# Kernel tuning notes

Measured on AMD Instinct MI355X. Metric: run time of the kernel, lower is better.

The kernel has to match this reference:

```python
import jax, jax.numpy as jnp
import numpy as np

B, T, D, H = 4, 2048, 1024, 16
HD = D // H  # 64
FF = 4 * D


def layernorm(x, g, b, eps=1e-5):
    mu = jnp.mean(x, axis=-1, keepdims=True)
    var = jnp.mean(jnp.square(x - mu), axis=-1, keepdims=True)
    return (x - mu) * jax.lax.rsqrt(var + eps) * g + b


def setup_inputs() -> dict:
    key = jax.random.key(0)
    ks = jax.random.split(key, 12)
    s_in = 1.0 / np.sqrt(D)
    s_ff = 1.0 / np.sqrt(FF)
    return {
        "x": jax.random.normal(ks[0], (B, T, D), dtype=jnp.float32),
        "mask": jnp.tril(jnp.ones((T, T), dtype=jnp.int32)),  # causal
        "ln1_g": jnp.ones((D,), jnp.float32),
        "ln1_b": jnp.zeros((D,), jnp.float32),
        "Wq": jax.random.uniform(ks[1], (H, D, HD), jnp.float32, -s_in, s_in),
        "bq": jnp.zeros((H, HD), jnp.float32),
        "Wk": jax.random.uniform(ks[2], (H, D, HD), jnp.float32, -s_in, s_in),
        "bk": jnp.zeros((H, HD), jnp.float32),
        "Wv": jax.random.uniform(ks[3], (H, D, HD), jnp.float32, -s_in, s_in),
        "bv": jnp.zeros((H, HD), jnp.float32),
        "Wo": jax.random.uniform(ks[4], (D, D), jnp.float32, -s_in, s_in),
        "bo": jnp.zeros((D,), jnp.float32),
        "ln2_g": jnp.ones((D,), jnp.float32),
        "ln2_b": jnp.zeros((D,), jnp.float32),
        "W1": jax.random.uniform(ks[5], (D, FF), jnp.float32, -s_in, s_in),
        "b1": jnp.zeros((FF,), jnp.float32),
        "W2": jax.random.uniform(ks[6], (FF, D), jnp.float32, -s_ff, s_ff),
        "b2": jnp.zeros((D,), jnp.float32),
    }


def reference(x, mask, ln1_g, ln1_b, Wq, bq, Wk, bk, Wv, bv, Wo, bo,
              ln2_g, ln2_b, W1, b1, W2, b2):
    # --- attention branch (dropout p=0, eval mode) ---
    h = layernorm(x, ln1_g, ln1_b)                      # [B,T,D]
    q = jnp.einsum('btd,hdk->bhtk', h, Wq) + bq[:, None, :]
    k = jnp.einsum('btd,hdk->bhtk', h, Wk) + bk[:, None, :]
    v = jnp.einsum('btd,hdk->bhtk', h, Wv) + bv[:, None, :]
    scores = jnp.einsum('bhqk,bhsk->bhqs', q, k) / jnp.sqrt(jnp.float32(HD))
    scores = jnp.where(mask == 0, -jnp.inf, scores)     # [B,H,T,T]
    attn = jax.nn.softmax(scores, axis=-1)
    ctx = jnp.einsum('bhqs,bhsk->bhqk', attn, v)        # [B,H,T,HD]
    # concat heads along feature dim (head order preserved)
    ctx = jnp.transpose(ctx, (0, 2, 1, 3)).reshape(x.shape[0], x.shape[1], D)
    attn_out = ctx @ Wo + bo
    x = x + attn_out
    # --- GELU FFN branch (torch nn.GELU default = exact erf) ---
    h2 = layernorm(x, ln2_g, ln2_b)
    ff = jax.nn.gelu(h2 @ W1 + b1, approximate=False) @ W2 + b2
    return x + ff
```

## Files before the change

### kernel.cpp

```cpp
#include <hip/hip_runtime.h>
#include <cstdint>
#include <cstddef>

typedef __bf16 bf16x8 __attribute__((ext_vector_type(8)));
typedef float  floatx4 __attribute__((ext_vector_type(4)));

__device__ __forceinline__ uint16_t f2b(float f) {
    uint32_t u = __builtin_bit_cast(uint32_t, f);
    return (uint16_t)((u + 0x7fffu + ((u >> 16) & 1)) >> 16);
}

__device__ __forceinline__ uint16_t bf16bits(float f) {
    __bf16 h = (__bf16)f;
    return __builtin_bit_cast(uint16_t, h);
}

__device__ __forceinline__ void gload_lds16(const void* g, void* l) {
    __builtin_amdgcn_global_load_lds(
        (__attribute__((address_space(1))) void*)(void*)g,
        (__attribute__((address_space(3))) void*)l, 16, 0, 0);
}

template<int CTRL>
__device__ __forceinline__ float dpp_rot(float v) {
    return __builtin_bit_cast(float,
        __builtin_amdgcn_update_dpp(0, __builtin_bit_cast(int, v),
                                    CTRL, 0xf, 0xf, true));
}
__device__ __forceinline__ float rowmax16(float v) {
    v = fmaxf(v, dpp_rot<0x128>(v));
    v = fmaxf(v, dpp_rot<0x124>(v));
    v = fmaxf(v, dpp_rot<0x122>(v));
    v = fmaxf(v, dpp_rot<0x121>(v));
    return v;
}
__device__ __forceinline__ float rowsum16(float v) {
    v += dpp_rot<0x128>(v);
    v += dpp_rot<0x124>(v);
    v += dpp_rot<0x122>(v);
    v += dpp_rot<0x121>(v);
    return v;
}

#define QSCALE 0.18033688011112042f

__global__ __launch_bounds__(256) void repack_qkv(
    const float* __restrict__ Wq, const float* __restrict__ Wk,
    const float* __restrict__ Wv, uint16_t* __restrict__ out)
{
    __shared__ uint16_t tile[32][33];
    const int m = blockIdx.z >> 4, h = blockIdx.z & 15;
    const float* W = (m == 0) ? Wq : (m == 1) ? Wk : Wv;
    const float scl = (m == 0) ? QSCALE : 1.0f;
    const float* src = W + (size_t)h * 1024 * 64;
    const int d0 = blockIdx.x * 32, hd0 = blockIdx.y * 32;
    const int tx = threadIdx.x & 31, ty = threadIdx.x >> 5;
#pragma unroll
    for (int i = 0; i < 4; ++i)
        tile[ty + i * 8][tx] = f2b(src[(size_t)(d0 + ty + i * 8) * 64 + hd0 + tx] * scl);
    __syncthreads();
    uint16_t* dst = out + (size_t)(m * 1024 + h * 64) * 1024;
#pragma unroll
    for (int i = 0; i < 4; ++i)
        dst[(size_t)(hd0 + ty + i * 8) * 1024 + d0 + tx] = tile[tx][ty + i * 8];
}

__global__ __launch_bounds__(256) void transpose_f2b(
    const float* __restrict__ in, uint16_t* __restrict__ out, int R, int C)
{
    __shared__ uint16_t tile[32][33];
    const int c0 = blockIdx.x * 32, r0 = blockIdx.y * 32;
    const int tx = threadIdx.x & 31, ty = threadIdx.x >> 5;
#pragma unroll
    for (int i = 0; i < 4; ++i)
        tile[ty + i * 8][tx] = f2b(in[(size_t)(r0 + ty + i * 8) * C + c0 + tx]);
    __syncthreads();
#pragma unroll
    for (int i = 0; i < 4; ++i)
        out[(size_t)(c0 + ty + i * 8) * R + r0 + tx] = tile[tx][ty + i * 8];
}

__global__ void concat_bias(const float* __restrict__ bq, const float* __restrict__ bk,
                            const float* __restrict__ bv, float* __restrict__ out)
{
    int i = blockIdx.x * 256 + threadIdx.x;
    out[i] = (i < 1024) ? bq[i] * QSCALE : (i < 2048) ? bk[i - 1024] : bv[i - 2048];
}

__global__ __launch_bounds__(256) void transpose_v(
    const uint16_t* __restrict__ qkv, uint16_t* __restrict__ Vt)
{
    __shared__ uint16_t tile[32][33];
    const int bh = blockIdx.z;
    const int b = bh >> 4, h = bh & 15;
    const int t0 = blockIdx.x * 32, hd0 = blockIdx.y * 32;
    const int tx = threadIdx.x & 31, ty = threadIdx.x >> 5;
    const uint16_t* src = qkv + (size_t)b * 2048 * 3072 + 2048 + h * 64;
#pragma unroll
    for (int i = 0; i < 4; ++i)
        tile[ty + i * 8][tx] = src[(size_t)(t0 + ty + i * 8) * 3072 + hd0 + tx];
    __syncthreads();
    uint16_t* dst = Vt + (size_t)bh * 64 * 2048;
#pragma unroll
    for (int i = 0; i < 4; ++i)
        dst[(size_t)(hd0 + ty + i * 8) * 2048 + t0 + tx] = tile[tx][ty + i * 8];
}

__global__ __launch_bounds__(256) void ln_bf16(
    const float* __restrict__ x, const float* __restrict__ g,
    const float* __restrict__ b, uint16_t* __restrict__ out)
{
    const int row = blockIdx.x;
    const int t = threadIdx.x;
    const float4 v = ((const float4*)(x + (size_t)row * 1024))[t];
    float s  = v.x + v.y + v.z + v.w;
    float s2 = v.x * v.x + v.y * v.y + v.z * v.z + v.w * v.w;
#pragma unroll
    for (int o = 32; o > 0; o >>= 1) { s += __shfl_down(s, o); s2 += __shfl_down(s2, o); }
    __shared__ float red[8];
    const int wave = t >> 6, lane = t & 63;
    if (lane == 0) { red[wave] = s; red[4 + wave] = s2; }
    __syncthreads();
    if (t == 0) {
        float a  = red[0] + red[1] + red[2] + red[3];
        float a2 = red[4] + red[5] + red[6] + red[7];
        float mu = a * (1.0f / 1024.0f);
        red[0] = mu;
        red[4] = rsqrtf(a2 * (1.0f / 1024.0f) - mu * mu + 1e-5f);
    }
    __syncthreads();
    const float mu = red[0], rs = red[4];
    const float4 gv = ((const float4*)g)[t];
    const float4 bv = ((const float4*)b)[t];
    ushort4 ov;
    ov.x = f2b((v.x - mu) * rs * gv.x + bv.x);
    ov.y = f2b((v.y - mu) * rs * gv.y + bv.y);
    ov.z = f2b((v.z - mu) * rs * gv.z + bv.z);
    ov.w = f2b((v.w - mu) * rs * gv.w + bv.w);
    ((ushort4*)(out + (size_t)row * 1024))[t] = ov;
}

__global__ __launch_bounds__(256, 3) void gemm_bf16(
    const uint16_t* __restrict__ A, const uint16_t* __restrict__ Bt,
    int M, int N, int K,
    const float* __restrict__ bias, const float* __restrict__ resid,
    float* __restrict__ outF, uint16_t* __restrict__ outB, int mode)
{
    __shared__ __align__(16) uint16_t lds[128 * 128];
    uint16_t* lA = lds;
    uint16_t* lB = lds + 128 * 64;
    const int tid  = threadIdx.x;
    const int wave = tid >> 6, lane = tid & 63;

    const int lid = (int)blockIdx.y * (int)gridDim.x + (int)blockIdx.x;
    const int xcd = lid & 7, t = lid >> 3;
    const int Mb = (M >> 7) >> 3;
    const int perChunk = Mb * 8;
    const int ch = t / perChunk, j = t - ch * perChunk;
    const int m0 = (xcd * Mb + (j & (Mb - 1))) * 128;
    const int n0 = (ch * 8 + (j / Mb)) * 128;

    const int wm = (wave >> 1) * 64, wn = (wave & 1) * 64;
    const int quad = lane >> 4, lrow = lane & 15;
    const int wbase = wave * 64;

    floatx4 acc[4][4] = {};

    const uint16_t* aT = A  + (size_t)m0 * K;
    const uint16_t* bT = Bt + (size_t)n0 * K;

    for (int k0 = 0; k0 < K; k0 += 64) {
        __syncthreads();
#pragma unroll
        for (int i = 0; i < 4; ++i) {
            const int cw = i * 256 + wbase;
            const int q  = cw + lane;
            const int row = q >> 3;
            const int g = ((q & 7) ^ (row & 7)) * 8;
            gload_lds16(aT + (size_t)row * K + k0 + g, &lA[cw * 8]);
            gload_lds16(bT + (size_t)row * K + k0 + g, &lB[cw * 8]);
        }
        __syncthreads();
        bf16x8 af[4][2], bfr[4][2];
#pragma unroll
        for (int mi = 0; mi < 4; ++mi) {
            const int rr = wm + mi * 16 + lrow;
#pragma unroll
            for (int hh = 0; hh < 2; ++hh)
                af[mi][hh] = *(const bf16x8*)
                    &lA[rr * 64 + (((hh * 4 + quad) ^ (rr & 7)) * 8)];
        }
#pragma unroll
        for (int ni = 0; ni < 4; ++ni) {
            const int rr = wn + ni * 16 + lrow;
#pragma unroll
            for (int hh = 0; hh < 2; ++hh)
                bfr[ni][hh] = *(const bf16x8*)
                    &lB[rr * 64 + (((hh * 4 + quad) ^ (rr & 7)) * 8)];
        }
#pragma unroll
        for (int mi = 0; mi < 4; ++mi)
#pragma unroll
            for (int ni = 0; ni < 4; ++ni) {
                acc[mi][ni] = __builtin_amdgcn_mfma_f32_16x16x32_bf16(
                    af[mi][0], bfr[ni][0], acc[mi][ni], 0, 0, 0);
                acc[mi][ni] = __builtin_amdgcn_mfma_f32_16x16x32_bf16(
                    af[mi][1], bfr[ni][1], acc[mi][ni], 0, 0, 0);
            }
    }

    __syncthreads();
    const int r0 = (lane >> 4) * 4;

    if (mode == 1) {
        float* cf = (float*)lds;
#pragma unroll
        for (int p = 0; p < 2; ++p) {
            if ((wave >> 1) == p) {
#pragma unroll
                for (int ni = 0; ni < 4; ++ni) {
                    const int col = wn + ni * 16 + lrow;
                    const float bv = bias[n0 + col];
#pragma unroll
                    for (int mi = 0; mi < 4; ++mi)
#pragma unroll
                        for (int r = 0; r < 4; ++r) {
                            const int row = mi * 16 + r0 + r;
                            const int g = (col >> 2) ^ (((row >> 2) & 1) << 2);
                            cf[row * 128 + g * 4 + (col & 3)] = acc[mi][ni][r] + bv;
                        }
                }
            }
            __syncthreads();
#pragma unroll
            for (int i = 0; i < 8; ++i) {
                const int ci = i * 256 + tid;
                const int row = ci >> 5, cg = ci & 31;
                const int g = cg ^ (((row >> 2) & 1) << 2);
                float4 v = *(const float4*)&cf[row * 128 + g * 4];
                const size_t gidx = (size_t)(m0 + p * 64 + row) * N + n0 + cg * 4;
                const float4 rz = *(const float4*)&resid[gidx];
                v.x += rz.x; v.y += rz.y; v.z += rz.z; v.w += rz.w;
                *(float4*)&outF[gidx] = v;
            }
            __syncthreads();
        }
    } else {
#pragma unroll
        for (int ni = 0; ni < 4; ++ni) {
            const int col = wn + ni * 16 + lrow;
            const float bv = bias[n0 + col];
#pragma unroll
            for (int mi = 0; mi < 4; ++mi)
#pragma unroll
                for (int r = 0; r < 4; ++r) {
                    const int row = wm + mi * 16 + r0 + r;
                    float v = acc[mi][ni][r] + bv;
                    if (mode == 2)
                        v = 0.5f * v * (1.0f + erff(v * 0.70710678118654752f));
                    const int g = (col >> 3) ^ (((row >> 2) & 3) << 1);
                    lds[row * 128 + g * 8 + (col & 7)] = bf16bits(v);
                }
        }
        __syncthreads();
#pragma unroll
        for (int i = 0; i < 8; ++i) {
            const int ci = i * 256 + tid;
            const int row = ci >> 4, cg = ci & 15;
            const int g = cg ^ (((row >> 2) & 3) << 1);
            const bf16x8 v = *(const bf16x8*)&lds[row * 128 + g * 8];
            *(bf16x8*)&outB[(size_t)(m0 + row) * N + n0 + cg * 8] = v;
        }
    }
}

__global__ __launch_bounds__(256, 2) void attn_kernel(
    const uint16_t* __restrict__ qkv, const uint16_t* __restrict__ Vt,
    uint16_t* __restrict__ ctx)
{
    const int h = blockIdx.y, b = blockIdx.z;
    const int tid = threadIdx.x, wave = tid >> 6, lane = tid & 63;
    const int quad = lane >> 4, lcol = lane & 15, lr4 = quad * 4;
    const int sx = lcol & 7;
    const uint16_t* qbase = qkv + (size_t)b * 2048 * 3072;
    const uint16_t* kgb = qbase + 1024 + h * 64;
    const uint16_t* vtb = Vt + (size_t)(b * 16 + h) * 64 * 2048;

    __shared__ __align__(16) uint16_t kbuf[2][64 * 64];
    __shared__ __align__(16) uint16_t vbuf[2][64 * 64];
    __shared__ __align__(16) uint16_t pshm[4][32 * 64];

    const int rr = lane >> 3, sl = lane & 7;
    const int swz = sl ^ rr;

#define STAGE(ktile, bb)                                                        \
    {                                                                           \
        const int _kb = (ktile) * 64;                                           \
        _Pragma("unroll")                                                       \
        for (int i = 0; i < 2; ++i) {                                           \
            const int j = wave * 2 + i;                                         \
            const int r = j * 8 + rr;                                           \
            gload_lds16(kgb + (size_t)(_kb + r) * 3072 + swz * 8,               \
                        &kbuf[bb][j * 512]);                                    \
            gload_lds16(vtb + (size_t)r * 2048 + _kb + swz * 8,                 \
                        &vbuf[bb][j * 512]);                                    \
        }                                                                       \
    }

    for (int pp = 0; pp < 2; ++pp) {
        const int qt = pp ? (int)blockIdx.x : 15 - (int)blockIdx.x;
        const int qr0 = qt * 128 + wave * 32;

        bf16x8 qf[2][2];
#pragma unroll
        for (int mi = 0; mi < 2; ++mi) {
            const uint16_t* qp = qbase + (size_t)(qr0 + mi * 16 + lcol) * 3072 + h * 64;
            qf[mi][0] = *(const bf16x8*)(qp + quad * 8);
            qf[mi][1] = *(const bf16x8*)(qp + 32 + quad * 8);
        }

        floatx4 o[2][4] = {};
        float m_i[2][4], l_i[2][4];
#pragma unroll
        for (int mi = 0; mi < 2; ++mi)
#pragma unroll
            for (int r = 0; r < 4; ++r) { m_i[mi][r] = -1e30f; l_i[mi][r] = 0.f; }

        const int nk = 2 * qt + 2;
        __syncthreads();
        STAGE(0, 0);
        int cur = 0;

        for (int kt = 0; kt < nk; ++kt) {
            const int kb = kt * 64;
            __syncthreads();
            if (kt + 1 < nk) STAGE(kt + 1, cur ^ 1);

            if (kb <= qr0 + 31) {
                bf16x8 kf[4][2];
#pragma unroll
                for (int nt = 0; nt < 4; ++nt) {
                    const int krow = nt * 16 + lcol;
                    kf[nt][0] = *(const bf16x8*)&kbuf[cur][krow * 64 + ((quad ^ sx) * 8)];
                    kf[nt][1] = *(const bf16x8*)&kbuf[cur][krow * 64 + (((quad + 4) ^ sx) * 8)];
                }
#pragma unroll
                for (int mi = 0; mi < 2; ++mi) {
                    floatx4 sv[4];
#pragma unroll
                    for (int nt = 0; nt < 4; ++nt) {
                        floatx4 s = {0.f, 0.f, 0.f, 0.f};
                        s = __builtin_amdgcn_mfma_f32_16x16x32_bf16(qf[mi][0], kf[nt][0], s, 0, 0, 0);
                        s = __builtin_amdgcn_mfma_f32_16x16x32_bf16(qf[mi][1], kf[nt][1], s, 0, 0, 0);
                        sv[nt] = s;
                    }
                    if (kb + 63 > qr0 + mi * 16) {
#pragma unroll
                        for (int nt = 0; nt < 4; ++nt)
#pragma unroll
                            for (int r = 0; r < 4; ++r) {
                                const int row = qr0 + mi * 16 + lr4 + r;
                                const int col = kb + nt * 16 + lcol;
                                if (col > row) sv[nt][r] = -1e30f;
                            }
                    }
#pragma unroll
                    for (int r = 0; r < 4; ++r) {
                        float m = fmaxf(fmaxf(sv[0][r], sv[1][r]),
                                        fmaxf(sv[2][r], sv[3][r]));
                        m = rowmax16(m);
                        const float mn = fmaxf(m_i[mi][r], m);
                        const float alpha = __builtin_amdgcn_exp2f(m_i[mi][r] - mn);
                        m_i[mi][r] = mn;
                        const int row = mi * 16 + lr4 + r;
                        const int rsw = row & 7;
                        float l = 0.f;
#pragma unroll
                        for (int nt = 0; nt < 4; ++nt) {
                            const float p = __builtin_amdgcn_exp2f(sv[nt][r] - mn);
                            l += p;
                            const int col = nt * 16 + lcol;
                            pshm[wave][row * 64 + (((col >> 3) ^ rsw) * 8) + (col & 7)] =
                                bf16bits(p);
                        }
                        l = rowsum16(l);
                        l_i[mi][r] = l_i[mi][r] * alpha + l;
#pragma unroll
                        for (int ht = 0; ht < 4; ++ht) o[mi][ht][r] *= alpha;
                    }
                }
                bf16x8 pf[2][2];
#pragma unroll
                for (int mi = 0; mi < 2; ++mi) {
                    const int prow = mi * 16 + lcol;
                    pf[mi][0] = *(const bf16x8*)&pshm[wave][prow * 64 + ((quad ^ sx) * 8)];
                    pf[mi][1] = *(const bf16x8*)&pshm[wave][prow * 64 + (((quad + 4) ^ sx) * 8)];
                }
#pragma unroll
                for (int ht = 0; ht < 4; ++ht) {
                    const int hd = ht * 16 + lcol;
                    const bf16x8 vf0 = *(const bf16x8*)&vbuf[cur][hd * 64 + ((quad ^ sx) * 8)];
                    const bf16x8 vf1 = *(const bf16x8*)&vbuf[cur][hd * 64 + (((quad + 4) ^ sx) * 8)];
#pragma unroll
                    for (int mi = 0; mi < 2; ++mi) {
                        o[mi][ht] = __builtin_amdgcn_mfma_f32_16x16x32_bf16(pf[mi][0], vf0, o[mi][ht], 0, 0, 0);
                        o[mi][ht] = __builtin_amdgcn_mfma_f32_16x16x32_bf16(pf[mi][1], vf1, o[mi][ht], 0, 0, 0);
                    }
                }
            }
            cur ^= 1;
        }

#pragma unroll
        for (int mi = 0; mi < 2; ++mi)
#pragma unroll
            for (int r = 0; r < 4; ++r) {
                const float inv = 1.0f / l_i[mi][r];
                const int row = qr0 + mi * 16 + lr4 + r;
#pragma unroll
                for (int ht = 0; ht < 4; ++ht)
                    ctx[(size_t)(b * 2048 + row) * 1024 + h * 64 + ht * 16 + lcol] =
                        bf16bits(o[mi][ht][r] * inv);
            }
    }
#undef STAGE
}

extern "C" void kernel_launch(void* const* d_in, const int* in_sizes, int n_in,
                              void* d_out, int out_size, void* d_ws, size_t ws_size,
                              hipStream_t stream)
{
    (void)in_sizes; (void)n_in; (void)out_size; (void)ws_size;
    const float* x     = (const float*)d_in[0];
    const float* ln1_g = (const float*)d_in[2];
    const float* ln1_b = (const float*)d_in[3];
    const float* Wq    = (const float*)d_in[4];
    const float* bq    = (const float*)d_in[5];
    const float* Wk    = (const float*)d_in[6];
    const float* bk    = (const float*)d_in[7];
    const float* Wv    = (const float*)d_in[8];
    const float* bv    = (const float*)d_in[9];
    const float* Wo    = (const float*)d_in[10];
    const float* bo    = (const float*)d_in[11];
    const float* ln2_g = (const float*)d_in[12];
    const float* ln2_b = (const float*)d_in[13];
    const float* W1    = (const float*)d_in[14];
    const float* b1    = (const float*)d_in[15];
    const float* W2    = (const float*)d_in[16];
    const float* b2    = (const float*)d_in[17];
    float* out = (float*)d_out;

    char* w = (char*)d_ws;
    uint16_t* Wqkv_t = (uint16_t*)w;  w += 6291456;
    uint16_t* Wo_t   = (uint16_t*)w;  w += 2097152;
    uint16_t* W1_t   = (uint16_t*)w;  w += 8388608;
    uint16_t* W2_t   = (uint16_t*)w;  w += 8388608;
    float*    bqkv   = (float*)w;     w += 16384;
    float*    x2     = (float*)w;     w += 33554432;
    char* region = w;
    uint16_t* hbuf = (uint16_t*)region;
    uint16_t* qkv  = (uint16_t*)(region + 16777216);
    uint16_t* Vt   = (uint16_t*)(region + 16777216 + 50331648);
    uint16_t* ctx  = hbuf;
    uint16_t* h2   = (uint16_t*)region;
    uint16_t* a1   = (uint16_t*)(region + 16777216);

    repack_qkv<<<dim3(32, 2, 48), 256, 0, stream>>>(Wq, Wk, Wv, Wqkv_t);
    transpose_f2b<<<dim3(32, 32),  256, 0, stream>>>(Wo, Wo_t, 1024, 1024);
    transpose_f2b<<<dim3(128, 32), 256, 0, stream>>>(W1, W1_t, 1024, 4096);
    transpose_f2b<<<dim3(32, 128), 256, 0, stream>>>(W2, W2_t, 4096, 1024);
    concat_bias<<<12, 256, 0, stream>>>(bq, bk, bv, bqkv);
    ln_bf16<<<8192, 256, 0, stream>>>(x, ln1_g, ln1_b, hbuf);
    gemm_bf16<<<dim3(24, 64), 256, 0, stream>>>(hbuf, Wqkv_t, 8192, 3072, 1024,
                                                bqkv, nullptr, nullptr, qkv, 0);
    transpose_v<<<dim3(64, 2, 64), 256, 0, stream>>>(qkv, Vt);
    attn_kernel<<<dim3(8, 16, 4), 256, 0, stream>>>(qkv, Vt, ctx);
    gemm_bf16<<<dim3(8, 64), 256, 0, stream>>>(ctx, Wo_t, 8192, 1024, 1024,
                                               bo, x, x2, nullptr, 1);
    ln_bf16<<<8192, 256, 0, stream>>>(x2, ln2_g, ln2_b, h2);
    gemm_bf16<<<dim3(32, 64), 256, 0, stream>>>(h2, W1_t, 8192, 4096, 1024,
                                                b1, nullptr, nullptr, a1, 2);
    gemm_bf16<<<dim3(8, 64), 256, 0, stream>>>(a1, W2_t, 8192, 1024, 4096,
                                               b2, x2, out, nullptr, 1);
}
```

Baseline: 538.3 us.

## Add 256x256 ping-pong GEMM for QKV and FFN1, prioritize MFMA in attention

Adds a new 512-thread GEMM kernel with 256x256 output tiles. It uses a double-buffered LDS pipeline with half-tile staging interleaved between MFMA phases, s_setprio around the MFMA bursts, and an XCD-aware block remap. This kernel replaces the 128-tile GEMM for the QKV projection and for the GELU FFN up-projection, raising arithmetic intensity and overlapping global-to-LDS loads with compute. The attention kernel also gets s_setprio around its MFMA blocks. The hand-scheduled barriers and vmcnt waits carry a risk of correctness or occupancy problems, since the kernel uses 128KB of LDS and a large accumulator register footprint.

```diff
diff --git a/kernel.cpp b/kernel.cpp
--- a/kernel.cpp
+++ b/kernel.cpp
@@ -273,6 +273,189 @@
         }
     }
 }
+
+#define CFENCE() asm volatile("" ::: "memory")
+#define BAR()   do { CFENCE(); __builtin_amdgcn_s_barrier(); CFENCE(); } while (0)
+#define LWAIT() do { asm volatile("s_waitcnt lgkmcnt(0)" ::: "memory");         \
+                     __builtin_amdgcn_sched_barrier(0); } while (0)
+#define GWAIT(N_) asm volatile("s_waitcnt vmcnt(" #N_ ")" ::: "memory")
+
+#define STAGE_HALF(SRC, DSTBASE, HALF, TILE)                                    \
+    { _Pragma("unroll")                                                         \
+      for (int _i = 0; _i < 2; ++_i) {                                          \
+        const int _q = _i * 512 + tid, _r = _q >> 3, _c = _q & 7;               \
+        gload_lds16(SRC + (size_t)((HALF) * 128 + _r) * K + (TILE) * 64         \
+                        + ((_c ^ (_r & 7)) * 8),                                \
+                    (DSTBASE) + (HALF) * 8192 + (_i * 512 + (wave << 6)) * 8);  \
+      } }
+
+#define TILE_BODY(TT, CUR)                                                      \
+  { const int _t = (TT);                                                        \
+    uint16_t* const lA  = sm + (CUR) * 16384;                                   \
+    uint16_t* const lB  = sm + 32768 + (CUR) * 16384;                           \
+    uint16_t* const lAn = sm + (1 - (CUR)) * 16384;                             \
+                                                                   \
+    _Pragma("unroll")                                                           \
+    for (int mi = 0; mi < 4; ++mi) {                                            \
+      const int rr = arow + mi * 16;                                            \
+      af[mi][0] = *(const bf16x8*)&lA[rr * 64 + c0];                            \
+      af[mi][1] = *(const bf16x8*)&lA[rr * 64 + c1];                            \
+    }                                                                           \
+    _Pragma("unroll")                                                           \
+    for (int ni = 0; ni < 4; ++ni) {                                            \
+      const int rb = brow + ni * 16;                                            \
+      bfr[ni][0] = *(const bf16x8*)&lB[rb * 64 + c0];                           \
+      bfr[ni][1] = *(const bf16x8*)&lB[rb * 64 + c1];                           \
+    }                                                                           \
+    if (_t + 1 < NT) { STAGE_HALF(aT, lAn, 1, _t + 1); }                        \
+    BAR(); LWAIT();                                                             \
+    __builtin_amdgcn_s_setprio(1);                                              \
+    _Pragma("unroll")                                                           \
+    for (int mi = 0; mi < 4; ++mi)                                              \
+      _Pragma("unroll")                                                         \
+      for (int ni = 0; ni < 2; ++ni) {                                          \
+        acc[mi][ni] = __builtin_amdgcn_mfma_f32_16x16x32_bf16(                  \
+            af[mi][0], bfr[ni][0], acc[mi][ni], 0, 0, 0);                       \
+        acc[mi][ni] = __builtin_amdgcn_mfma_f32_16x16x32_bf16(                  \
+            af[mi][1], bfr[ni][1], acc[mi][ni], 0, 0, 0);                       \
+      }                                                                         \
+    __builtin_amdgcn_s_setprio(0);                                              \
+    BAR();                                                                      \
+                                                                   \
+    if (_t + 2 < NT) { STAGE_HALF(bT, lB, 0, _t + 2); }                         \
+    BAR();                                                                      \
+    __builtin_amdgcn_s_setprio(1);                                              \
+    _Pragma("unroll")                                                           \
+    for (int mi = 0; mi < 4; ++mi)                                              \
+      _Pragma("unroll")                                                         \
+      for (int ni = 2; ni < 4; ++ni) {                                          \
+        acc[mi][ni] = __builtin_amdgcn_mfma_f32_16x16x32_bf16(                  \
+            af[mi][0], bfr[ni][0], acc[mi][ni], 0, 0, 0);                       \
+        acc[mi][ni] = __builtin_amdgcn_mfma_f32_16x16x32_bf16(                  \
+            af[mi][1], bfr[ni][1], acc[mi][ni], 0, 0, 0);                       \
+      }                                                                         \
+    __builtin_amdgcn_s_setprio(0);                                              \
+    BAR();                                                                      \
+                                                                   \
+    _Pragma("unroll")                                                           \
+    for (int mi = 0; mi < 4; ++mi) {                                            \
+      const int rr = arow + 64 + mi * 16;                                       \
+      af[mi][0] = *(const bf16x8*)&lA[rr * 64 + c0];                            \
+      af[mi][1] = *(const bf16x8*)&lA[rr * 64 + c1];                            \
+    }                                                                           \
+    if (_t + 2 < NT) { STAGE_HALF(bT, lB, 1, _t + 2); }                         \
+    BAR(); LWAIT();                                                             \
+    __builtin_amdgcn_s_setprio(1);                                              \
+    _Pragma("unroll")                                                           \
+    for (int mi = 0; mi < 4; ++mi)                                              \
+      _Pragma("unroll")                                                         \
+      for (int ni = 0; ni < 2; ++ni) {                                          \
+        acc[mi + 4][ni] = __builtin_amdgcn_mfma_f32_16x16x32_bf16(              \
+            af[mi][0], bfr[ni][0], acc[mi + 4][ni], 0, 0, 0);                   \
+        acc[mi + 4][ni] = __builtin_amdgcn_mfma_f32_16x16x32_bf16(              \
+            af[mi][1], bfr[ni][1], acc[mi + 4][ni], 0, 0, 0);                   \
+      }                                                                         \
+    __builtin_amdgcn_s_setprio(0);                                              \
+    BAR();                                                                      \
+                                                                   \
+    if (_t + 2 < NT) { STAGE_HALF(aT, lA, 0, _t + 2); }                         \
+    BAR();                                                                      \
+    __builtin_amdgcn_s_setprio(1);                                              \
+    _Pragma("unroll")                                                           \
+    for (int mi = 0; mi < 4; ++mi)                                              \
+      _Pragma("unroll")                                                         \
+      for (int ni = 2; ni < 4; ++ni) {                                          \
+        acc[mi + 4][ni] = __builtin_amdgcn_mfma_f32_16x16x32_bf16(              \
+            af[mi][0], bfr[ni][0], acc[mi + 4][ni], 0, 0, 0);                   \
+        acc[mi + 4][ni] = __builtin_amdgcn_mfma_f32_16x16x32_bf16(              \
+            af[mi][1], bfr[ni][1], acc[mi + 4][ni], 0, 0, 0);                   \
+      }                                                                         \
+    __builtin_amdgcn_s_setprio(0);                                              \
+    if (_t + 2 < NT) { GWAIT(6); } else { GWAIT(0); }                           \
+    BAR();                                                                      \
+  }
+
+template<int GELU>
+__global__ __launch_bounds__(512, 2) void gemm256(
+    const uint16_t* __restrict__ A, const uint16_t* __restrict__ Bt,
+    int M, int N, int K,
+    const float* __restrict__ bias, uint16_t* __restrict__ outB)
+{
+    (void)M;
+    __shared__ __align__(16) uint16_t sm[65536];
+    const int tid  = threadIdx.x;
+    const int wave = tid >> 6, lane = tid & 63;
+    const int quad = lane >> 4, lcol = lane & 15, sx = lcol & 7;
+    const int wm = wave >> 2, wn = wave & 3;
+
+    const int nwg = (int)gridDim.x;
+    const int q8  = nwg >> 3;
+    const int wg  = ((int)blockIdx.x & 7) * q8 + ((int)blockIdx.x >> 3);
+    const int ntn = N >> 8;
+    const int tm = wg / ntn, tn = wg - tm * ntn;
+    const int m0 = tm * 256, n0 = tn * 256;
+
+    const uint16_t* aT = A  + (size_t)m0 * K;
+    const uint16_t* bT = Bt + (size_t)n0 * K;
+    const int NT = K >> 6;
+
+    const int arow = wm * 128 + lcol;
+    const int brow = wn * 64  + lcol;
+    const int c0 = (quad ^ sx) * 8, c1 = ((quad + 4) ^ sx) * 8;
+
+    floatx4 acc[8][4] = {};
+    bf16x8 af[4][2], bfr[4][2];
+
+    uint16_t* const lA0 = sm;
+    uint16_t* const lA1 = sm + 16384;
+    uint16_t* const lB0 = sm + 32768;
+    uint16_t* const lB1 = sm + 49152;
+
+    STAGE_HALF(bT, lB0, 0, 0);
+    STAGE_HALF(bT, lB0, 1, 0);
+    STAGE_HALF(aT, lA0, 0, 0);
+    STAGE_HALF(aT, lA0, 1, 0);
+    GWAIT(4);
+    STAGE_HALF(bT, lB1, 0, 1);
+    STAGE_HALF(bT, lB1, 1, 1);
+    STAGE_HALF(aT, lA1, 0, 1);
+    GWAIT(6);
+    BAR();
+
+    for (int t = 0; t < NT; t += 2) {
+        TILE_BODY(t, 0);
+        TILE_BODY(t + 1, 1);
+    }
+
+#pragma unroll
+    for (int ni = 0; ni < 4; ++ni) {
+        const int col = wn * 64 + ni * 16 + lcol;
+        const float bv = bias[n0 + col];
+#pragma unroll
+        for (int mi = 0; mi < 8; ++mi)
+#pragma unroll
+            for (int r = 0; r < 4; ++r) {
+                const int row = wm * 128 + mi * 16 + quad * 4 + r;
+                float v = acc[mi][ni][r] + bv;
+                if (GELU)
+                    v = 0.5f * v * (1.0f + erff(v * 0.70710678118654752f));
+                const int g = (col >> 3) ^ (((row >> 2) & 3) << 1);
+                sm[row * 256 + g * 8 + (col & 7)] = bf16bits(v);
+            }
+    }
+    __syncthreads();
+#pragma unroll
+    for (int it = 0; it < 16; ++it) {
+        const int ci = it * 512 + tid;
+        const int row = ci >> 5, cg = ci & 31;
+        const int g = cg ^ (((row >> 2) & 3) << 1);
+        const bf16x8 v = *(const bf16x8*)&sm[row * 256 + g * 8];
+        *(bf16x8*)&outB[(size_t)(m0 + row) * N + n0 + cg * 8] = v;
+    }
+}
+
+#undef TILE_BODY
+#undef STAGE_HALF
 
 __global__ __launch_bounds__(256, 2) void attn_kernel(
     const uint16_t* __restrict__ qkv, const uint16_t* __restrict__ Vt,
@@ -347,6 +530,7 @@
 #pragma unroll
                 for (int mi = 0; mi < 2; ++mi) {
                     floatx4 sv[4];
+                    __builtin_amdgcn_s_setprio(1);
 #pragma unroll
                     for (int nt = 0; nt < 4; ++nt) {
                         floatx4 s = {0.f, 0.f, 0.f, 0.f};
@@ -354,6 +538,7 @@
                         s = __builtin_amdgcn_mfma_f32_16x16x32_bf16(qf[mi][1], kf[nt][1], s, 0, 0, 0);
                         sv[nt] = s;
                     }
+                    __builtin_amdgcn_s_setprio(0);
                     if (kb + 63 > qr0 + mi * 16) {
 #pragma unroll
                         for (int nt = 0; nt < 4; ++nt)
@@ -396,6 +581,7 @@
                     pf[mi][0] = *(const bf16x8*)&pshm[wave][prow * 64 + ((quad ^ sx) * 8)];
                     pf[mi][1] = *(const bf16x8*)&pshm[wave][prow * 64 + (((quad + 4) ^ sx) * 8)];
                 }
+                __builtin_amdgcn_s_setprio(1);
 #pragma unroll
                 for (int ht = 0; ht < 4; ++ht) {
                     const int hd = ht * 16 + lcol;
@@ -407,6 +593,7 @@
                         o[mi][ht] = __builtin_amdgcn_mfma_f32_16x16x32_bf16(pf[mi][1], vf1, o[mi][ht], 0, 0, 0);
                     }
                 }
+                __builtin_amdgcn_s_setprio(0);
             }
             cur ^= 1;
         }
@@ -471,15 +658,15 @@
     transpose_f2b<<<dim3(32, 128), 256, 0, stream>>>(W2, W2_t, 4096, 1024);
     concat_bias<<<12, 256, 0, stream>>>(bq, bk, bv, bqkv);
     ln_bf16<<<8192, 256, 0, stream>>>(x, ln1_g, ln1_b, hbuf);
-    gemm_bf16<<<dim3(24, 64), 256, 0, stream>>>(hbuf, Wqkv_t, 8192, 3072, 1024,
-                                                bqkv, nullptr, nullptr, qkv, 0);
+    gemm256<0><<<dim3(384), 512, 0, stream>>>(hbuf, Wqkv_t, 8192, 3072, 1024,
+                                              bqkv, qkv);
     transpose_v<<<dim3(64, 2, 64), 256, 0, stream>>>(qkv, Vt);
     attn_kernel<<<dim3(8, 16, 4), 256, 0, stream>>>(qkv, Vt, ctx);
     gemm_bf16<<<dim3(8, 64), 256, 0, stream>>>(ctx, Wo_t, 8192, 1024, 1024,
                                                bo, x, x2, nullptr, 1);
     ln_bf16<<<8192, 256, 0, stream>>>(x2, ln2_g, ln2_b, h2);
-    gemm_bf16<<<dim3(32, 64), 256, 0, stream>>>(h2, W1_t, 8192, 4096, 1024,
-                                                b1, nullptr, nullptr, a1, 2);
+    gemm256<1><<<dim3(512), 512, 0, stream>>>(h2, W1_t, 8192, 4096, 1024,
+                                              b1, a1);
     gemm_bf16<<<dim3(8, 64), 256, 0, stream>>>(a1, W2_t, 8192, 1024, 4096,
                                                b2, x2, out, nullptr, 1);
 }
```

Result: no change. 546.7 us (+1.6%).
